# Kernel optimization log

Hardware: AMD Instinct MI355X
Metric: run time of the kernel (lower is better)

## Reference

```python
import jax, jax.numpy as jnp
import numpy as np

N = 50000   # nodes
E = 600000  # edges
D = 128     # in_channels
H = 32      # MLP hidden


def setup_inputs() -> dict:
    key = jax.random.key(0)
    ks = jax.random.split(key, 10)
    x = jax.random.normal(ks[0], (N, D), dtype=jnp.float32)
    edge_index = jax.random.randint(ks[1], (2, E), 0, N, dtype=jnp.int32)
    W_gcn = jax.random.normal(ks[2], (D, D), dtype=jnp.float32) / np.sqrt(D)
    b_gcn = jnp.zeros((D,), dtype=jnp.float32)
    w1 = jax.random.normal(ks[3], (D, H), dtype=jnp.float32) / np.sqrt(D)
    b1 = jnp.zeros((H,), dtype=jnp.float32)
    w2 = jax.random.normal(ks[4], (H, H), dtype=jnp.float32) / np.sqrt(H)
    b2 = jnp.zeros((H,), dtype=jnp.float32)
    w3 = jax.random.normal(ks[5], (H, 1), dtype=jnp.float32) / np.sqrt(H)
    b3 = jnp.zeros((1,), dtype=jnp.float32)
    return {"x": x, "edge_index": edge_index, "W_gcn": W_gcn, "b_gcn": b_gcn,
            "w1": w1, "b1": b1, "w2": w2, "b2": b2, "w3": w3, "b3": b3}


def _gcn_conv(x, edge_index, W, b):
    """PyG GCNConv: add self-loops, symmetric D^-1/2 (A+I) D^-1/2 normalization."""
    xw = x @ W  # [N, D]
    loop = jnp.arange(N, dtype=edge_index.dtype)
    row = jnp.concatenate([edge_index[0], loop])  # source
    col = jnp.concatenate([edge_index[1], loop])  # target
    deg = jax.ops.segment_sum(jnp.ones_like(col, dtype=xw.dtype), col, num_segments=N)
    dinv = jnp.where(deg > 0, jax.lax.rsqrt(deg), 0.0)
    norm = dinv[row] * dinv[col]              # [E+N]
    msg = xw[row] * norm[:, None]             # gather + scale, [E+N, D]
    out = jax.ops.segment_sum(msg, col, num_segments=N)  # scatter-add, [N, D]
    return out + b


def reference(x, edge_index, W_gcn, b_gcn, w1, b1, w2, b2, w3, b3):
    out = jax.nn.relu(_gcn_conv(x, edge_index, W_gcn, b_gcn))
    h = out + x                               # residual
    h = jax.nn.relu(h @ w1 + b1)
    h = jax.nn.relu(h @ w2 + b2)
    return h @ w3 + b3                        # [N, 1]
```

## Files before the change

### kernel.cpp

```cpp
#include <hip/hip_runtime.h>

#define DIM 128
#define HID 32
#define CAP 64

typedef __attribute__((ext_vector_type(8))) short v8s;
typedef __attribute__((ext_vector_type(8))) unsigned short v8u;
typedef __attribute__((ext_vector_type(4))) float v4f;

static __device__ __forceinline__ unsigned short f2bf(float f) {
    unsigned int u = __float_as_uint(f);
    u += 0x7fffu + ((u >> 16) & 1u);
    return (unsigned short)(u >> 16);
}

__global__ __launch_bounds__(256) void prep_kernel(int* __restrict__ cnt,
                                                   const float* __restrict__ W,
                                                   unsigned short* __restrict__ wbt,
                                                   int n, int nz) {
    int t = threadIdx.x;
    if ((int)blockIdx.x < nz) {
        int i0 = (blockIdx.x << 10) + t * 4;
        if (i0 + 3 < n) {
            *(int4*)&cnt[i0] = make_int4(0, 0, 0, 0);
        } else {
            for (int i = i0; i < n; ++i) cnt[i] = 0;
        }
    } else {
        int base = (blockIdx.x - nz) * 2048 + t * 8;
#pragma unroll
        for (int i = 0; i < 8; ++i) {
            int f = base + i;
            int k = f >> 7, nn = f & 127;
            wbt[nn * 128 + k] = f2bf(W[f]);
        }
    }
}

__global__ __launch_bounds__(256) void gemm_fill_kernel(const float* __restrict__ x,
                                                        const unsigned short* __restrict__ wbt,
                                                        signed char* __restrict__ xwq,
                                                        float* __restrict__ sc,
                                                        const int* __restrict__ ei,
                                                        int* __restrict__ cnt,
                                                        int* __restrict__ srcs,
                                                        int n, int E, int ngemm) {
    __shared__ __attribute__((aligned(16))) unsigned short wt[128 * 136];
    __shared__ __attribute__((aligned(16))) unsigned short xs[64 * 136];
    int t = threadIdx.x;
    if ((int)blockIdx.x < ngemm) {
        int row0 = blockIdx.x * 64;
#pragma unroll
        for (int i = 0; i < 8; ++i) {
            int u = t + i * 256;
            int nn = u >> 4;
            int kk = (u & 15) * 8;
            *(v8u*)&wt[nn * 136 + kk] = *(const v8u*)&wbt[nn * 128 + kk];
        }
#pragma unroll
        for (int i = 0; i < 4; ++i) {
            int u = t + i * 256;
            int rl = u >> 4;
            int kk = (u & 15) * 8;
            float4 qa = make_float4(0.f, 0.f, 0.f, 0.f), qb = qa;
            if (row0 + rl < n) {
                const float4* src = (const float4*)(x + (size_t)(row0 + rl) * DIM + kk);
                qa = src[0]; qb = src[1];
            }
            v8u pk;
            pk[0] = f2bf(qa.x); pk[1] = f2bf(qa.y); pk[2] = f2bf(qa.z); pk[3] = f2bf(qa.w);
            pk[4] = f2bf(qb.x); pk[5] = f2bf(qb.y); pk[6] = f2bf(qb.z); pk[7] = f2bf(qb.w);
            *(v8u*)&xs[rl * 136 + kk] = pk;
        }
        __syncthreads();

        int w = t >> 6;
        int l = t & 63;
        int q = l >> 4;
        int mn = l & 15;
        v8s afrag[4];
#pragma unroll
        for (int kt = 0; kt < 4; ++kt)
            afrag[kt] = *(const v8s*)&xs[(w * 16 + mn) * 136 + kt * 32 + q * 8];
        v4f acc[8];
#pragma unroll
        for (int ct = 0; ct < 8; ++ct) {
            acc[ct] = (v4f){0.f, 0.f, 0.f, 0.f};
#pragma unroll
            for (int kt = 0; kt < 4; ++kt) {
                v8s bfrag = *(const v8s*)&wt[(ct * 16 + mn) * 136 + kt * 32 + q * 8];
                acc[ct] = __builtin_amdgcn_mfma_f32_16x16x32_bf16(afrag[kt], bfrag, acc[ct], 0, 0, 0);
            }
        }
        float m[4];
#pragma unroll
        for (int i = 0; i < 4; ++i) {
            float mm = 0.f;
#pragma unroll
            for (int ct = 0; ct < 8; ++ct) mm = fmaxf(mm, fabsf(acc[ct][i]));
            m[i] = mm;
        }
#pragma unroll
        for (int off = 1; off < 16; off <<= 1) {
#pragma unroll
            for (int i = 0; i < 4; ++i) m[i] = fmaxf(m[i], __shfl_xor(m[i], off));
        }
        float inv[4];
#pragma unroll
        for (int i = 0; i < 4; ++i) {
            m[i] = fmaxf(m[i], 1e-20f);
            inv[i] = 127.0f / m[i];
        }
        if (mn == 0) {
#pragma unroll
            for (int i = 0; i < 4; ++i) {
                int rowg = row0 + w * 16 + q * 4 + i;
                if (rowg < n) sc[rowg] = m[i] * (1.0f / 127.0f);
            }
        }
#pragma unroll
        for (int ct = 0; ct < 8; ++ct) {
            int colg = ct * 16 + mn;
#pragma unroll
            for (int i = 0; i < 4; ++i) {
                int rowg = row0 + w * 16 + q * 4 + i;
                if (rowg < n)
                    xwq[(size_t)rowg * DIM + colg] =
                        (signed char)__float2int_rn(acc[ct][i] * inv[i]);
            }
        }
    } else {
        const int* col = ei + E;
        int base = ((blockIdx.x - ngemm) * 256 + t) * 4;
        if (base + 3 < E) {
            int4 r4 = *(const int4*)&ei[base];
            int4 c4 = *(const int4*)&col[base];
            int p0 = atomicAdd(&cnt[c4.x], 1);
            int p1 = atomicAdd(&cnt[c4.y], 1);
            int p2 = atomicAdd(&cnt[c4.z], 1);
            int p3 = atomicAdd(&cnt[c4.w], 1);
            if (p0 < CAP) srcs[(c4.x << 6) + p0] = r4.x;
            if (p1 < CAP) srcs[(c4.y << 6) + p1] = r4.y;
            if (p2 < CAP) srcs[(c4.z << 6) + p2] = r4.z;
            if (p3 < CAP) srcs[(c4.w << 6) + p3] = r4.w;
        } else {
            for (int e = base; e < E; ++e) {
                int r = ei[e], c = col[e];
                int p = atomicAdd(&cnt[c], 1);
                if (p < CAP) srcs[(c << 6) + p] = r;
            }
        }
    }
}

__global__ __launch_bounds__(256) void dw_kernel(const int* __restrict__ cnt,
                                                 const float* __restrict__ sc,
                                                 float* __restrict__ dw, int n) {
    int i0 = (blockIdx.x * 256 + threadIdx.x) * 4;
    if (i0 + 3 < n) {
        int4 c4 = *(const int4*)&cnt[i0];
        float4 s4 = *(const float4*)&sc[i0];
        float4 w4;
        w4.x = rsqrtf((float)c4.x + 1.0f) * s4.x;
        w4.y = rsqrtf((float)c4.y + 1.0f) * s4.y;
        w4.z = rsqrtf((float)c4.z + 1.0f) * s4.z;
        w4.w = rsqrtf((float)c4.w + 1.0f) * s4.w;
        *(float4*)&dw[i0] = w4;
    } else {
        for (int i = i0; i < n; ++i) dw[i] = rsqrtf((float)cnt[i] + 1.0f) * sc[i];
    }
}

__global__ __launch_bounds__(256) void gather_tail_kernel(
    const signed char* __restrict__ xwq, const float* __restrict__ x,
    const int* __restrict__ cnt, const int* __restrict__ srcs,
    const float* __restrict__ dw, const float* __restrict__ sc,
    const float* __restrict__ b_gcn,
    const float* __restrict__ w1, const float* __restrict__ b1,
    const float* __restrict__ w2, const float* __restrict__ b2,
    const float* __restrict__ w3, const float* __restrict__ b3,
    float* __restrict__ out, int n) {
    __shared__ float hs[8][132];
    __shared__ float t1s[8][40];
    int t = threadIdx.x;
    int g = t >> 5, j = t & 31;
    int node = blockIdx.x * 8 + g;

    if (node < n) {
        int d = min(cnt[node], CAP);
        int beg = node << 6;
        int aq = ((const int*)(xwq + (size_t)node * DIM))[j];
        float scn = sc[node];
        float4 xv = ((const float4*)(x + (size_t)node * DIM))[j];
        float4 bg = ((const float4*)b_gcn)[j];
        float ax = 0.f, ay = 0.f, az = 0.f, aw = 0.f;
        for (int c0 = 0; c0 < d; c0 += 32) {
            int sj = 0; float wj = 0.f;
            if (c0 + j < d) {
                sj = srcs[beg + c0 + j];
                wj = dw[sj];
            }
            int m = min(32, d - c0);
            int i = 0;
            for (; i + 8 <= m; i += 8) {
                int v[8]; float wgt[8];
#pragma unroll
                for (int u = 0; u < 8; ++u) {
                    int src = __shfl(sj, i + u, 32);
                    wgt[u] = __shfl(wj, i + u, 32);
                    v[u] = ((const int*)(xwq + (size_t)src * DIM))[j];
                }
#pragma unroll
                for (int u = 0; u < 8; ++u) {
                    ax += wgt[u] * (float)((v[u] << 24) >> 24);
                    ay += wgt[u] * (float)((v[u] << 16) >> 24);
                    az += wgt[u] * (float)((v[u] <<  8) >> 24);
                    aw += wgt[u] * (float)( v[u]        >> 24);
                }
            }
            for (; i + 4 <= m; i += 4) {
                int v[4]; float wgt[4];
#pragma unroll
                for (int u = 0; u < 4; ++u) {
                    int src = __shfl(sj, i + u, 32);
                    wgt[u] = __shfl(wj, i + u, 32);
                    v[u] = ((const int*)(xwq + (size_t)src * DIM))[j];
                }
#pragma unroll
                for (int u = 0; u < 4; ++u) {
                    ax += wgt[u] * (float)((v[u] << 24) >> 24);
                    ay += wgt[u] * (float)((v[u] << 16) >> 24);
                    az += wgt[u] * (float)((v[u] <<  8) >> 24);
                    aw += wgt[u] * (float)( v[u]        >> 24);
                }
            }
            for (; i < m; ++i) {
                int src = __shfl(sj, i, 32);
                float w = __shfl(wj, i, 32);
                int v0 = ((const int*)(xwq + (size_t)src * DIM))[j];
                ax += w * (float)((v0 << 24) >> 24);
                ay += w * (float)((v0 << 16) >> 24);
                az += w * (float)((v0 <<  8) >> 24);
                aw += w * (float)( v0        >> 24);
            }
        }
        float di = rsqrtf((float)d + 1.0f);
        float sself = di * di * scn;
        float* h = &hs[g][4 * j];
        h[0] = fmaxf(di * ax + sself * (float)((aq << 24) >> 24) + bg.x, 0.f) + xv.x;
        h[1] = fmaxf(di * ay + sself * (float)((aq << 16) >> 24) + bg.y, 0.f) + xv.y;
        h[2] = fmaxf(di * az + sself * (float)((aq <<  8) >> 24) + bg.z, 0.f) + xv.z;
        h[3] = fmaxf(di * aw + sself * (float)( aq        >> 24) + bg.w, 0.f) + xv.w;
        float acc = b1[j];
        for (int k = 0; k < DIM; k += 4) {
            float4 hv = *(const float4*)&hs[g][k];
            acc += hv.x * w1[(k + 0) * HID + j];
            acc += hv.y * w1[(k + 1) * HID + j];
            acc += hv.z * w1[(k + 2) * HID + j];
            acc += hv.w * w1[(k + 3) * HID + j];
        }
        t1s[g][j] = fmaxf(acc, 0.0f);
        acc = b2[j];
        for (int k = 0; k < HID; k += 4) {
            float4 tv = *(const float4*)&t1s[g][k];
            acc += tv.x * w2[(k + 0) * HID + j];
            acc += tv.y * w2[(k + 1) * HID + j];
            acc += tv.z * w2[(k + 2) * HID + j];
            acc += tv.w * w2[(k + 3) * HID + j];
        }
        float v = fmaxf(acc, 0.0f) * w3[j];
#pragma unroll
        for (int off = 16; off > 0; off >>= 1) v += __shfl_down(v, off, 32);
        if (j == 0) out[node] = v + b3[0];
    }
}

extern "C" void kernel_launch(void* const* d_in, const int* in_sizes, int n_in,
                              void* d_out, int out_size, void* d_ws, size_t ws_size,
                              hipStream_t stream) {
    const float* x     = (const float*)d_in[0];
    const int*   ei    = (const int*)d_in[1];
    const float* W_gcn = (const float*)d_in[2];
    const float* b_gcn = (const float*)d_in[3];
    const float* w1    = (const float*)d_in[4];
    const float* b1    = (const float*)d_in[5];
    const float* w2    = (const float*)d_in[6];
    const float* b2    = (const float*)d_in[7];
    const float* w3    = (const float*)d_in[8];
    const float* b3    = (const float*)d_in[9];
    float* out = (float*)d_out;

    const int n = in_sizes[0] / DIM;
    const int E = in_sizes[1] / 2;

    char* ws = (char*)d_ws;
    signed char* xwq = (signed char*)ws;
    char* p = ws + (size_t)n * DIM;
    p = (char*)(((size_t)p + 15) & ~(size_t)15);
    float* sc   = (float*)p;         p += (size_t)n * sizeof(float);
    float* dw   = (float*)p;         p += (size_t)n * sizeof(float);
    int*   cnt  = (int*)p;           p += (size_t)n * sizeof(int);
    p = (char*)(((size_t)p + 255) & ~(size_t)255);
    int*   srcs = (int*)p;           p += (size_t)n * CAP * sizeof(int);
    unsigned short* wbt = (unsigned short*)p;

    const int nz     = (n + 1023) / 1024;
    const int ngemm  = (n + 63) / 64;
    const int nfill  = (E + 1023) / 1024;

    prep_kernel<<<nz + 8, 256, 0, stream>>>(cnt, W_gcn, wbt, n, nz);
    gemm_fill_kernel<<<ngemm + nfill, 256, 0, stream>>>(x, wbt, xwq, sc, ei,
                                                        cnt, srcs, n, E, ngemm);
    dw_kernel<<<(n + 1023) / 1024, 256, 0, stream>>>(cnt, sc, dw, n);
    gather_tail_kernel<<<(n + 7) / 8, 256, 0, stream>>>(xwq, x, cnt, srcs, dw, sc,
                                                        b_gcn, w1, b1, w2, b2,
                                                        w3, b3, out, n);
}
```

Before: 181.3 us.

## Drop LDS staging in fused GEMM/fill kernel and schedule fill blocks first

Removes the 52KB shared-memory staging of W and the x tile from the GEMM path. Each lane now loads and converts its A fragment straight from global x, and B fragments are read directly from the transposed bf16 weight in global/L2, with launch bounds asking for 4 blocks per CU. The edge-bucketing fill blocks are reordered to come first so the atomic-heavy work starts early, and each thread now handles 8 edges instead of 4. The aim is higher occupancy and overlap of the scatter with the GEMM. The cost is redundant global/L2 reads of W across waves.

```diff
diff --git a/kernel.cpp b/kernel.cpp
--- a/kernel.cpp
+++ b/kernel.cpp
@@ -37,61 +37,82 @@
     }
 }
 
-__global__ __launch_bounds__(256) void gemm_fill_kernel(const float* __restrict__ x,
-                                                        const unsigned short* __restrict__ wbt,
-                                                        signed char* __restrict__ xwq,
-                                                        float* __restrict__ sc,
-                                                        const int* __restrict__ ei,
-                                                        int* __restrict__ cnt,
-                                                        int* __restrict__ srcs,
-                                                        int n, int E, int ngemm) {
-    __shared__ __attribute__((aligned(16))) unsigned short wt[128 * 136];
-    __shared__ __attribute__((aligned(16))) unsigned short xs[64 * 136];
+__global__ __launch_bounds__(256, 4) void gemm_fill_kernel(const float* __restrict__ x,
+                                                           const unsigned short* __restrict__ wbt,
+                                                           signed char* __restrict__ xwq,
+                                                           float* __restrict__ sc,
+                                                           const int* __restrict__ ei,
+                                                           int* __restrict__ cnt,
+                                                           int* __restrict__ srcs,
+                                                           int n, int E, int nfill) {
     int t = threadIdx.x;
-    if ((int)blockIdx.x < ngemm) {
-        int row0 = blockIdx.x * 64;
-#pragma unroll
-        for (int i = 0; i < 8; ++i) {
-            int u = t + i * 256;
-            int nn = u >> 4;
-            int kk = (u & 15) * 8;
-            *(v8u*)&wt[nn * 136 + kk] = *(const v8u*)&wbt[nn * 128 + kk];
-        }
-#pragma unroll
-        for (int i = 0; i < 4; ++i) {
-            int u = t + i * 256;
-            int rl = u >> 4;
-            int kk = (u & 15) * 8;
-            float4 qa = make_float4(0.f, 0.f, 0.f, 0.f), qb = qa;
-            if (row0 + rl < n) {
-                const float4* src = (const float4*)(x + (size_t)(row0 + rl) * DIM + kk);
-                qa = src[0]; qb = src[1];
-            }
-            v8u pk;
-            pk[0] = f2bf(qa.x); pk[1] = f2bf(qa.y); pk[2] = f2bf(qa.z); pk[3] = f2bf(qa.w);
-            pk[4] = f2bf(qb.x); pk[5] = f2bf(qb.y); pk[6] = f2bf(qb.z); pk[7] = f2bf(qb.w);
-            *(v8u*)&xs[rl * 136 + kk] = pk;
-        }
-        __syncthreads();
-
+    if ((int)blockIdx.x < nfill) {
+        const int* col = ei + E;
+        int base = ((int)blockIdx.x * 256 + t) * 8;
+        if (base + 7 < E) {
+            int4 ra = *(const int4*)&ei[base];
+            int4 rb = *(const int4*)&ei[base + 4];
+            int4 ca = *(const int4*)&col[base];
+            int4 cb = *(const int4*)&col[base + 4];
+            int p0 = atomicAdd(&cnt[ca.x], 1);
+            int p1 = atomicAdd(&cnt[ca.y], 1);
+            int p2 = atomicAdd(&cnt[ca.z], 1);
+            int p3 = atomicAdd(&cnt[ca.w], 1);
+            int p4 = atomicAdd(&cnt[cb.x], 1);
+            int p5 = atomicAdd(&cnt[cb.y], 1);
+            int p6 = atomicAdd(&cnt[cb.z], 1);
+            int p7 = atomicAdd(&cnt[cb.w], 1);
+            if (p0 < CAP) srcs[(ca.x << 6) + p0] = ra.x;
+            if (p1 < CAP) srcs[(ca.y << 6) + p1] = ra.y;
+            if (p2 < CAP) srcs[(ca.z << 6) + p2] = ra.z;
+            if (p3 < CAP) srcs[(ca.w << 6) + p3] = ra.w;
+            if (p4 < CAP) srcs[(cb.x << 6) + p4] = rb.x;
+            if (p5 < CAP) srcs[(cb.y << 6) + p5] = rb.y;
+            if (p6 < CAP) srcs[(cb.z << 6) + p6] = rb.z;
+            if (p7 < CAP) srcs[(cb.w << 6) + p7] = rb.w;
+        } else {
+            for (int e = base; e < E; ++e) {
+                int r = ei[e], c = col[e];
+                int p = atomicAdd(&cnt[c], 1);
+                if (p < CAP) srcs[(c << 6) + p] = r;
+            }
+        }
+    } else {
+        int row0 = ((int)blockIdx.x - nfill) * 64;
         int w = t >> 6;
         int l = t & 63;
         int q = l >> 4;
         int mn = l & 15;
+        int row = row0 + w * 16 + mn;
+
         v8s afrag[4];
-#pragma unroll
-        for (int kt = 0; kt < 4; ++kt)
-            afrag[kt] = *(const v8s*)&xs[(w * 16 + mn) * 136 + kt * 32 + q * 8];
+        const float* xr = x + (size_t)row * DIM + q * 8;
+#pragma unroll
+        for (int kt = 0; kt < 4; ++kt) {
+            float4 qa = make_float4(0.f, 0.f, 0.f, 0.f), qb = qa;
+            if (row < n) {
+                const float4* s4 = (const float4*)(xr + kt * 32);
+                qa = s4[0];
+                qb = s4[1];
+            }
+            v8u pk;
+            pk[0] = f2bf(qa.x); pk[1] = f2bf(qa.y); pk[2] = f2bf(qa.z); pk[3] = f2bf(qa.w);
+            pk[4] = f2bf(qb.x); pk[5] = f2bf(qb.y); pk[6] = f2bf(qb.z); pk[7] = f2bf(qb.w);
+            afrag[kt] = (v8s)pk;
+        }
+
         v4f acc[8];
+        const unsigned short* wr = wbt + mn * 128 + q * 8;
 #pragma unroll
         for (int ct = 0; ct < 8; ++ct) {
             acc[ct] = (v4f){0.f, 0.f, 0.f, 0.f};
 #pragma unroll
             for (int kt = 0; kt < 4; ++kt) {
-                v8s bfrag = *(const v8s*)&wt[(ct * 16 + mn) * 136 + kt * 32 + q * 8];
+                v8s bfrag = *(const v8s*)(wr + ct * (16 * 128) + kt * 32);
                 acc[ct] = __builtin_amdgcn_mfma_f32_16x16x32_bf16(afrag[kt], bfrag, acc[ct], 0, 0, 0);
             }
         }
+
         float m[4];
 #pragma unroll
         for (int i = 0; i < 4; ++i) {
@@ -127,27 +148,6 @@
                 if (rowg < n)
                     xwq[(size_t)rowg * DIM + colg] =
                         (signed char)__float2int_rn(acc[ct][i] * inv[i]);
-            }
-        }
-    } else {
-        const int* col = ei + E;
-        int base = ((blockIdx.x - ngemm) * 256 + t) * 4;
-        if (base + 3 < E) {
-            int4 r4 = *(const int4*)&ei[base];
-            int4 c4 = *(const int4*)&col[base];
-            int p0 = atomicAdd(&cnt[c4.x], 1);
-            int p1 = atomicAdd(&cnt[c4.y], 1);
-            int p2 = atomicAdd(&cnt[c4.z], 1);
-            int p3 = atomicAdd(&cnt[c4.w], 1);
-            if (p0 < CAP) srcs[(c4.x << 6) + p0] = r4.x;
-            if (p1 < CAP) srcs[(c4.y << 6) + p1] = r4.y;
-            if (p2 < CAP) srcs[(c4.z << 6) + p2] = r4.z;
-            if (p3 < CAP) srcs[(c4.w << 6) + p3] = r4.w;
-        } else {
-            for (int e = base; e < E; ++e) {
-                int r = ei[e], c = col[e];
-                int p = atomicAdd(&cnt[c], 1);
-                if (p < CAP) srcs[(c << 6) + p] = r;
             }
         }
     }
@@ -306,11 +306,11 @@
 
     const int nz     = (n + 1023) / 1024;
     const int ngemm  = (n + 63) / 64;
-    const int nfill  = (E + 1023) / 1024;
+    const int nfill  = (E + 2047) / 2048;
 
     prep_kernel<<<nz + 8, 256, 0, stream>>>(cnt, W_gcn, wbt, n, nz);
-    gemm_fill_kernel<<<ngemm + nfill, 256, 0, stream>>>(x, wbt, xwq, sc, ei,
-                                                        cnt, srcs, n, E, ngemm);
+    gemm_fill_kernel<<<nfill + ngemm, 256, 0, stream>>>(x, wbt, xwq, sc, ei,
+                                                        cnt, srcs, n, E, nfill);
     dw_kernel<<<(n + 1023) / 1024, 256, 0, stream>>>(cnt, sc, dw, n);
     gather_tail_kernel<<<(n + 7) / 8, 256, 0, stream>>>(xwq, x, cnt, srcs, dw, sc,
                                                         b_gcn, w1, b1, w2, b2,
```

New measurement: 178.3 us. About the same (-1.6%).
